# Performance work log

Measured on AMD Instinct MI355X. Metric: run time of the kernel, lower is better.

## Reference

```python
import jax, jax.numpy as jnp
import numpy as np

IN_SIZE = 4096
OUT_SIZE = 4096
BATCH = 256
NNZ = (IN_SIZE * OUT_SIZE) // 2


def setup_inputs() -> dict:
    key = jax.random.key(0)
    k_x, k_row, k_col, k_val = jax.random.split(key, 4)
    X = jax.random.normal(k_x, (BATCH, IN_SIZE), dtype=jnp.float32)
    rows = jax.random.randint(k_row, (NNZ,), 0, IN_SIZE, dtype=jnp.int64)
    cols = jax.random.randint(k_col, (NNZ,), 0, OUT_SIZE, dtype=jnp.int64)
    idx = jnp.stack([rows, cols], axis=1)  # [NNZ, 2] (input_idx, output_idx)
    lim = 1.0 / np.sqrt(IN_SIZE)
    val = jax.random.uniform(k_val, (NNZ,), dtype=jnp.float32, minval=-lim, maxval=lim)
    bias = jnp.zeros((OUT_SIZE,), dtype=jnp.float32)
    return {"X": X, "idx": idx, "val": val, "bias": bias}


def reference(X, idx, val, bias):
    # Scatter the COO sparse weight into a dense [IN, OUT] matrix.
    # .add accumulates duplicate indices, matching tf.SparseTensor matmul semantics.
    W = jnp.zeros((IN_SIZE, OUT_SIZE), dtype=val.dtype).at[idx[:, 0], idx[:, 1]].add(val)
    # Z = X @ W + b  (original: transpose(sparse_matmul(W^T, X^T)) + b)
    Z = jnp.dot(X, W) + bias
    return jax.nn.relu(Z)
```

## Files before the change

kernel.cpp:

```cpp
#include <hip/hip_runtime.h>
#include <hip/hip_bf16.h>

#define IN_SIZE 4096
#define OUT_SIZE 4096
#define BATCH 256
#define NNZ ((IN_SIZE * OUT_SIZE) / 2)

#define NB    512
#define BBIN  1024
#define EPB   (NNZ / BBIN)
#define CHUNK 4096
#define NCH   (EPB / CHUNK)
#define REP    8
#define SUBCAP 3072
#define CAP    (REP * SUBCAP)
#define SPLITK 4

#define BM 64
#define BN 64
#define BK 64
#define LDA 72

typedef float f32x4 __attribute__((ext_vector_type(4)));
typedef short s16x8 __attribute__((ext_vector_type(8)));

static const size_t OFF_XBF  = 0;
static const size_t OFF_WTBF = (size_t)2 << 20;
static const size_t OFF_PART = (size_t)34 << 20;
static const size_t OFF_BIN  = (size_t)50 << 20;
static const size_t OFF_CNT  = (size_t)98 << 20;
static const size_t WS_NEED  = OFF_CNT + (size_t)REP * NB * 4;

__device__ __forceinline__ short bfbits(float f) {
    __hip_bfloat16 h = __float2bfloat16(f);
    return __builtin_bit_cast(short, h);
}
__device__ __forceinline__ s16x8 pack8(f32x4 lo, f32x4 hi) {
    s16x8 r;
    r[0] = bfbits(lo[0]); r[1] = bfbits(lo[1]); r[2] = bfbits(lo[2]); r[3] = bfbits(lo[3]);
    r[4] = bfbits(hi[0]); r[5] = bfbits(hi[1]); r[6] = bfbits(hi[2]); r[7] = bfbits(hi[3]);
    return r;
}
__device__ __forceinline__ unsigned packel(int r, int c, float v) {
    return ((unsigned)(unsigned short)bfbits(v) << 15) |
           (unsigned)((c & 7) * IN_SIZE + r);
}
__device__ __forceinline__ float unpackv(unsigned p) {
    return __uint_as_float((p >> 15) << 16);
}

__device__ __forceinline__ void scan512(const unsigned* h, unsigned* out,
                                        unsigned* wsum, int t) {
    const int lane = t & 63, wid = t >> 6;
    const unsigned a0 = h[2 * t], a1 = h[2 * t + 1];
    const unsigned s = a0 + a1;
    unsigned inc = s;
#pragma unroll
    for (int d = 1; d < 64; d <<= 1) {
        const unsigned n = __shfl_up(inc, d);
        if (lane >= d) inc += n;
    }
    if (lane == 63) wsum[wid] = inc;
    __syncthreads();
    unsigned wpre = 0;
#pragma unroll
    for (int i = 0; i < 4; ++i)
        if (i < wid) wpre += wsum[i];
    const unsigned ex = wpre + inc - s;
    out[2 * t]     = ex;
    out[2 * t + 1] = ex + a0;
    __syncthreads();
}

__global__ __launch_bounds__(256) void k_xcvt(const float* __restrict__ X,
                                              s16x8* __restrict__ Xb) {
    const int i8 = blockIdx.x * 256 + threadIdx.x;
    const f32x4 lo = reinterpret_cast<const f32x4*>(X)[2 * i8];
    const f32x4 hi = reinterpret_cast<const f32x4*>(X)[2 * i8 + 1];
    Xb[i8] = pack8(lo, hi);
}

__global__ __launch_bounds__(256) void k_bin(const int4* __restrict__ idx4,
                                             const float2* __restrict__ val2,
                                             unsigned* __restrict__ cnt,
                                             unsigned* __restrict__ binned) {
    __shared__ unsigned hist[NB], start[NB], curb[NB], wsum[4];
    __shared__ uint2 st[CHUNK];
    const int t = threadIdx.x, blk = blockIdx.x;
    const int rep = blk & (REP - 1);

    for (int ch = 0; ch < NCH; ++ch) {
        hist[2 * t] = 0; hist[2 * t + 1] = 0;
        __syncthreads();
        const int pbase = (blk * EPB + ch * CHUNK) / 2;
        unsigned eb[16], er[16], epk[16];
#pragma unroll
        for (int j = 0; j < 8; ++j) {
            const int4 e   = idx4[pbase + t + 256 * j];
            const float2 v = val2[pbase + t + 256 * j];
            eb[2 * j]      = ((unsigned)e.y) >> 3;
            epk[2 * j]     = packel(e.x, e.y, v.x);
            er[2 * j]      = atomicAdd(&hist[eb[2 * j]], 1u);
            eb[2 * j + 1]  = ((unsigned)e.w) >> 3;
            epk[2 * j + 1] = packel(e.z, e.w, v.y);
            er[2 * j + 1]  = atomicAdd(&hist[eb[2 * j + 1]], 1u);
        }
        __syncthreads();
        scan512(hist, start, wsum, t);
        {
            const unsigned h0 = hist[2 * t], h1 = hist[2 * t + 1];
            const unsigned r0 = h0 ? atomicAdd(&cnt[rep * NB + 2 * t], h0) : 0u;
            const unsigned r1 = h1 ? atomicAdd(&cnt[rep * NB + 2 * t + 1], h1) : 0u;
            curb[2 * t]     = (unsigned)(2 * t) * CAP + rep * SUBCAP + r0;
            curb[2 * t + 1] = (unsigned)(2 * t + 1) * CAP + rep * SUBCAP + r1;
        }
        __syncthreads();
#pragma unroll
        for (int j = 0; j < 16; ++j) {
            const unsigned lp = start[eb[j]] + er[j];
            st[lp] = make_uint2(curb[eb[j]] + er[j], epk[j]);
        }
        __syncthreads();
#pragma unroll
        for (int j = 0; j < 16; ++j) {
            const uint2 s = st[t + 256 * j];
            binned[s.x] = s.y;
        }
        __syncthreads();
    }
}

__global__ __launch_bounds__(1024) void k_accum(const unsigned* __restrict__ binned,
                                                const unsigned* __restrict__ cnt,
                                                s16x8* __restrict__ Wtb8) {
    __shared__ float acc[8 * IN_SIZE];
    const int t = threadIdx.x, b = blockIdx.x;
    f32x4* a4 = reinterpret_cast<f32x4*>(acc);
#pragma unroll
    for (int j = 0; j < (8 * IN_SIZE / 4) / 1024; ++j)
        a4[t + 1024 * j] = (f32x4){0.f, 0.f, 0.f, 0.f};
    __syncthreads();
    const unsigned base = (unsigned)b * CAP;
#pragma unroll 1
    for (int r = 0; r < REP; ++r) {
        const unsigned n  = cnt[r * NB + b];
        const unsigned rb = base + r * SUBCAP;
        for (unsigned i = t; i < n; i += 1024) {
            const unsigned p = binned[rb + i];
            atomicAdd(&acc[p & 32767u], unpackv(p));
        }
    }
    __syncthreads();
    s16x8* dst = Wtb8 + (size_t)b * (8 * IN_SIZE / 8);
#pragma unroll
    for (int j = 0; j < (8 * IN_SIZE / 8) / 1024; ++j) {
        const int i8 = t + 1024 * j;
        dst[i8] = pack8(a4[2 * i8], a4[2 * i8 + 1]);
    }
}

__global__ __launch_bounds__(256) void k_gemm(const short* __restrict__ A,
                                              const short* __restrict__ B,
                                              float* __restrict__ part) {
    __shared__ short As[BM * LDA];
    __shared__ short Bs[BN * LDA];
    const int t  = threadIdx.x;
    const int l  = t & 63;
    const int w  = t >> 6;
    const int wm = (w >> 1) * 32, wn = (w & 1) * 32;
    const int lr = l & 15, kg = (l >> 4) * 8;
    const int bn = blockIdx.x * BN, bm = blockIdx.y * BM;
    const size_t kb = (size_t)blockIdx.z * (IN_SIZE / SPLITK);

    const int r0s = t >> 3;
    const int r1s = r0s + 32;
    const int c0  = (t & 7) * 8;
    const short* gA0 = A + (size_t)(bm + r0s) * IN_SIZE + kb + c0;
    const short* gA1 = A + (size_t)(bm + r1s) * IN_SIZE + kb + c0;
    const short* gB0 = B + (size_t)(bn + r0s) * IN_SIZE + kb + c0;
    const short* gB1 = B + (size_t)(bn + r1s) * IN_SIZE + kb + c0;

    f32x4 acc[2][2] = {};
    s16x8 ra0 = *reinterpret_cast<const s16x8*>(gA0);
    s16x8 ra1 = *reinterpret_cast<const s16x8*>(gA1);
    s16x8 rb0 = *reinterpret_cast<const s16x8*>(gB0);
    s16x8 rb1 = *reinterpret_cast<const s16x8*>(gB1);

    const int NIT = (IN_SIZE / SPLITK) / BK;
#pragma unroll 1
    for (int it = 0; it < NIT; ++it) {
        __syncthreads();
        *reinterpret_cast<s16x8*>(&As[r0s * LDA + c0]) = ra0;
        *reinterpret_cast<s16x8*>(&As[r1s * LDA + c0]) = ra1;
        *reinterpret_cast<s16x8*>(&Bs[r0s * LDA + c0]) = rb0;
        *reinterpret_cast<s16x8*>(&Bs[r1s * LDA + c0]) = rb1;
        __syncthreads();
        if (it + 1 < NIT) {
            const int o = (it + 1) * BK;
            ra0 = *reinterpret_cast<const s16x8*>(gA0 + o);
            ra1 = *reinterpret_cast<const s16x8*>(gA1 + o);
            rb0 = *reinterpret_cast<const s16x8*>(gB0 + o);
            rb1 = *reinterpret_cast<const s16x8*>(gB1 + o);
        }
        s16x8 af[2][2], bf[2][2];
#pragma unroll
        for (int kk = 0; kk < 2; ++kk) {
#pragma unroll
            for (int mi = 0; mi < 2; ++mi)
                af[kk][mi] = *reinterpret_cast<const s16x8*>(
                    &As[(wm + mi * 16 + lr) * LDA + kk * 32 + kg]);
#pragma unroll
            for (int ni = 0; ni < 2; ++ni)
                bf[kk][ni] = *reinterpret_cast<const s16x8*>(
                    &Bs[(wn + ni * 16 + lr) * LDA + kk * 32 + kg]);
        }
#pragma unroll
        for (int kk = 0; kk < 2; ++kk)
#pragma unroll
            for (int mi = 0; mi < 2; ++mi)
#pragma unroll
                for (int ni = 0; ni < 2; ++ni)
                    acc[mi][ni] = __builtin_amdgcn_mfma_f32_16x16x32_bf16(
                        af[kk][mi], bf[kk][ni], acc[mi][ni], 0, 0, 0);
    }

    float* P = part + (size_t)blockIdx.z * (BATCH * OUT_SIZE);
#pragma unroll
    for (int mi = 0; mi < 2; ++mi)
#pragma unroll
        for (int ni = 0; ni < 2; ++ni) {
            const int col = bn + wn + ni * 16 + lr;
            const int r0 = bm + wm + mi * 16 + ((l >> 4) << 2);
#pragma unroll
            for (int rr = 0; rr < 4; ++rr)
                P[(size_t)(r0 + rr) * OUT_SIZE + col] = acc[mi][ni][rr];
        }
}

__global__ __launch_bounds__(256) void k_reduce(const float* __restrict__ part,
                                                const float* __restrict__ bias,
                                                float* __restrict__ Z) {
    const int i4 = blockIdx.x * 256 + threadIdx.x;
    f32x4 s = reinterpret_cast<const f32x4*>(part)[i4];
#pragma unroll
    for (int r = 1; r < SPLITK; ++r) {
        const f32x4 p = reinterpret_cast<const f32x4*>(part + (size_t)r * BATCH * OUT_SIZE)[i4];
#pragma unroll
        for (int k = 0; k < 4; ++k) s[k] += p[k];
    }
    const f32x4 bv = reinterpret_cast<const f32x4*>(bias)[i4 & (OUT_SIZE / 4 - 1)];
    f32x4 o;
#pragma unroll
    for (int k = 0; k < 4; ++k) o[k] = fmaxf(s[k] + bv[k], 0.f);
    reinterpret_cast<f32x4*>(Z)[i4] = o;
}

#define SC_BLOCKS 1024
__global__ __launch_bounds__(256) void scatter_t(const int2* __restrict__ idx2,
                                                 const float* __restrict__ val,
                                                 float* __restrict__ Wt) {
    const int stride = SC_BLOCKS * 256;
    int i = blockIdx.x * 256 + threadIdx.x;
#pragma unroll 1
    for (int iter = 0; iter < NNZ / (4 * SC_BLOCKS * 256); ++iter) {
        const int2 e0 = idx2[i];
        const int2 e1 = idx2[i + stride];
        const int2 e2 = idx2[i + 2 * stride];
        const int2 e3 = idx2[i + 3 * stride];
        const float v0 = val[i], v1 = val[i + stride], v2 = val[i + 2 * stride], v3 = val[i + 3 * stride];
        atomicAdd(&Wt[e0.y * IN_SIZE + e0.x], v0);
        atomicAdd(&Wt[e1.y * IN_SIZE + e1.x], v1);
        atomicAdd(&Wt[e2.y * IN_SIZE + e2.x], v2);
        atomicAdd(&Wt[e3.y * IN_SIZE + e3.x], v3);
        i += 4 * stride;
    }
}

__global__ __launch_bounds__(256) void gemm_mfma(const float* __restrict__ X,
                                                 const float* __restrict__ Wt,
                                                 const float* __restrict__ bias,
                                                 float* __restrict__ Z) {
    const int l = threadIdx.x & 63, w = threadIdx.x >> 6;
    const int bm = blockIdx.y * 128, bn = blockIdx.x * 32;
    const int lr = l & 15, kg = (l >> 4) * 8;
    const float* pA[2];
    const float* pB[2];
#pragma unroll
    for (int mi = 0; mi < 2; ++mi) pA[mi] = X + (bm + w * 32 + mi * 16 + lr) * IN_SIZE + kg;
#pragma unroll
    for (int ni = 0; ni < 2; ++ni) pB[ni] = Wt + (bn + ni * 16 + lr) * IN_SIZE + kg;
    f32x4 acc[2][2] = {};
#pragma unroll 2
    for (int k0 = 0; k0 < IN_SIZE; k0 += 32) {
        s16x8 a[2], b[2];
#pragma unroll
        for (int mi = 0; mi < 2; ++mi) {
            const f32x4 lo = *reinterpret_cast<const f32x4*>(pA[mi]);
            const f32x4 hi = *reinterpret_cast<const f32x4*>(pA[mi] + 4);
            a[mi] = pack8(lo, hi); pA[mi] += 32;
        }
#pragma unroll
        for (int ni = 0; ni < 2; ++ni) {
            const f32x4 lo = *reinterpret_cast<const f32x4*>(pB[ni]);
            const f32x4 hi = *reinterpret_cast<const f32x4*>(pB[ni] + 4);
            b[ni] = pack8(lo, hi); pB[ni] += 32;
        }
#pragma unroll
        for (int mi = 0; mi < 2; ++mi)
#pragma unroll
            for (int ni = 0; ni < 2; ++ni)
                acc[mi][ni] = __builtin_amdgcn_mfma_f32_16x16x32_bf16(a[mi], b[ni], acc[mi][ni], 0, 0, 0);
    }
#pragma unroll
    for (int mi = 0; mi < 2; ++mi)
#pragma unroll
        for (int ni = 0; ni < 2; ++ni) {
            const int col = bn + ni * 16 + lr;
            const float bv = bias[col];
            const int r0 = bm + w * 32 + mi * 16 + ((l >> 4) << 2);
#pragma unroll
            for (int rr = 0; rr < 4; ++rr)
                Z[(r0 + rr) * OUT_SIZE + col] = fmaxf(acc[mi][ni][rr] + bv, 0.f);
        }
}

extern "C" void kernel_launch(void* const* d_in, const int* in_sizes, int n_in,
                              void* d_out, int out_size, void* d_ws, size_t ws_size,
                              hipStream_t stream) {
    const float* X    = (const float*)d_in[0];
    const int*   idx  = (const int*)d_in[1];
    const float* val  = (const float*)d_in[2];
    const float* bias = (const float*)d_in[3];
    float* Z = (float*)d_out;
    char*  ws = (char*)d_ws;

    if (ws_size >= WS_NEED) {
        s16x8*    Xb     = (s16x8*)(ws + OFF_XBF);
        short*    Wtb    = (short*)(ws + OFF_WTBF);
        float*    part   = (float*)(ws + OFF_PART);
        unsigned* binned = (unsigned*)(ws + OFF_BIN);
        unsigned* cnt    = (unsigned*)(ws + OFF_CNT);

        hipMemsetAsync(cnt, 0, (size_t)REP * NB * 4, stream);
        k_xcvt<<<(BATCH * IN_SIZE) / (256 * 8), 256, 0, stream>>>(X, Xb);
        k_bin<<<BBIN, 256, 0, stream>>>((const int4*)idx, (const float2*)val, cnt, binned);
        k_accum<<<NB, 1024, 0, stream>>>(binned, cnt, (s16x8*)Wtb);
        dim3 gg(OUT_SIZE / BN, BATCH / BM, SPLITK);
        k_gemm<<<gg, 256, 0, stream>>>((const short*)Xb, Wtb, part);
        k_reduce<<<(BATCH * OUT_SIZE) / (256 * 4), 256, 0, stream>>>(part, bias, Z);
    } else {
        float* Wt = (float*)d_ws;
        hipMemsetAsync(Wt, 0, (size_t)IN_SIZE * OUT_SIZE * sizeof(float), stream);
        scatter_t<<<SC_BLOCKS, 256, 0, stream>>>((const int2*)idx, val, Wt);
        dim3 grid(OUT_SIZE / 32, BATCH / 128);
        gemm_mfma<<<grid, 256, 0, stream>>>(X, Wt, bias, Z);
    }
}
```

Baseline: 227.3 us.

## Fuse X bf16 conversion into GEMM and double bin count with fixed-unroll accumulation

```diff
diff --git a/kernel.cpp b/kernel.cpp
--- a/kernel.cpp
+++ b/kernel.cpp
@@ -6,13 +6,14 @@
 #define BATCH 256
 #define NNZ ((IN_SIZE * OUT_SIZE) / 2)
 
-#define NB    512
+#define NB    1024
 #define BBIN  1024
+#define BTHR  512
 #define EPB   (NNZ / BBIN)
 #define CHUNK 4096
 #define NCH   (EPB / CHUNK)
 #define REP    8
-#define SUBCAP 3072
+#define SUBCAP 1536
 #define CAP    (REP * SUBCAP)
 #define SPLITK 4
 
@@ -24,11 +25,10 @@
 typedef float f32x4 __attribute__((ext_vector_type(4)));
 typedef short s16x8 __attribute__((ext_vector_type(8)));
 
-static const size_t OFF_XBF  = 0;
-static const size_t OFF_WTBF = (size_t)2 << 20;
-static const size_t OFF_PART = (size_t)34 << 20;
-static const size_t OFF_BIN  = (size_t)50 << 20;
-static const size_t OFF_CNT  = (size_t)98 << 20;
+static const size_t OFF_WTBF = 0;
+static const size_t OFF_PART = (size_t)32 << 20;
+static const size_t OFF_BIN  = (size_t)48 << 20;
+static const size_t OFF_CNT  = (size_t)96 << 20;
 static const size_t WS_NEED  = OFF_CNT + (size_t)REP * NB * 4;
 
 __device__ __forceinline__ short bfbits(float f) {
@@ -42,15 +42,15 @@
     return r;
 }
 __device__ __forceinline__ unsigned packel(int r, int c, float v) {
-    return ((unsigned)(unsigned short)bfbits(v) << 15) |
-           (unsigned)((c & 7) * IN_SIZE + r);
+    return ((unsigned)(unsigned short)bfbits(v) << 14) |
+           (unsigned)((c & 3) * IN_SIZE + r);
 }
 __device__ __forceinline__ float unpackv(unsigned p) {
-    return __uint_as_float((p >> 15) << 16);
-}
-
-__device__ __forceinline__ void scan512(const unsigned* h, unsigned* out,
-                                        unsigned* wsum, int t) {
+    return __uint_as_float((p >> 14) << 16);
+}
+
+__device__ __forceinline__ void scan1024(const unsigned* h, unsigned* out,
+                                         unsigned* wsum, int t) {
     const int lane = t & 63, wid = t >> 6;
     const unsigned a0 = h[2 * t], a1 = h[2 * t + 1];
     const unsigned s = a0 + a1;
@@ -64,7 +64,7 @@
     __syncthreads();
     unsigned wpre = 0;
 #pragma unroll
-    for (int i = 0; i < 4; ++i)
+    for (int i = 0; i < 8; ++i)
         if (i < wid) wpre += wsum[i];
     const unsigned ex = wpre + inc - s;
     out[2 * t]     = ex;
@@ -72,19 +72,11 @@
     __syncthreads();
 }
 
-__global__ __launch_bounds__(256) void k_xcvt(const float* __restrict__ X,
-                                              s16x8* __restrict__ Xb) {
-    const int i8 = blockIdx.x * 256 + threadIdx.x;
-    const f32x4 lo = reinterpret_cast<const f32x4*>(X)[2 * i8];
-    const f32x4 hi = reinterpret_cast<const f32x4*>(X)[2 * i8 + 1];
-    Xb[i8] = pack8(lo, hi);
-}
-
-__global__ __launch_bounds__(256) void k_bin(const int4* __restrict__ idx4,
-                                             const float2* __restrict__ val2,
-                                             unsigned* __restrict__ cnt,
-                                             unsigned* __restrict__ binned) {
-    __shared__ unsigned hist[NB], start[NB], curb[NB], wsum[4];
+__global__ __launch_bounds__(BTHR) void k_bin(const int4* __restrict__ idx4,
+                                              const float2* __restrict__ val2,
+                                              unsigned* __restrict__ cnt,
+                                              unsigned* __restrict__ binned) {
+    __shared__ unsigned hist[NB], start[NB], curb[NB], wsum[8];
     __shared__ uint2 st[CHUNK];
     const int t = threadIdx.x, blk = blockIdx.x;
     const int rep = blk & (REP - 1);
@@ -93,20 +85,20 @@
         hist[2 * t] = 0; hist[2 * t + 1] = 0;
         __syncthreads();
         const int pbase = (blk * EPB + ch * CHUNK) / 2;
-        unsigned eb[16], er[16], epk[16];
-#pragma unroll
-        for (int j = 0; j < 8; ++j) {
-            const int4 e   = idx4[pbase + t + 256 * j];
-            const float2 v = val2[pbase + t + 256 * j];
-            eb[2 * j]      = ((unsigned)e.y) >> 3;
+        unsigned eb[8], er[8], epk[8];
+#pragma unroll
+        for (int j = 0; j < 4; ++j) {
+            const int4 e   = idx4[pbase + t + BTHR * j];
+            const float2 v = val2[pbase + t + BTHR * j];
+            eb[2 * j]      = ((unsigned)e.y) >> 2;
             epk[2 * j]     = packel(e.x, e.y, v.x);
             er[2 * j]      = atomicAdd(&hist[eb[2 * j]], 1u);
-            eb[2 * j + 1]  = ((unsigned)e.w) >> 3;
+            eb[2 * j + 1]  = ((unsigned)e.w) >> 2;
             epk[2 * j + 1] = packel(e.z, e.w, v.y);
             er[2 * j + 1]  = atomicAdd(&hist[eb[2 * j + 1]], 1u);
         }
         __syncthreads();
-        scan512(hist, start, wsum, t);
+        scan1024(hist, start, wsum, t);
         {
             const unsigned h0 = hist[2 * t], h1 = hist[2 * t + 1];
             const unsigned r0 = h0 ? atomicAdd(&cnt[rep * NB + 2 * t], h0) : 0u;
@@ -116,14 +108,14 @@
         }
         __syncthreads();
 #pragma unroll
-        for (int j = 0; j < 16; ++j) {
+        for (int j = 0; j < 8; ++j) {
             const unsigned lp = start[eb[j]] + er[j];
             st[lp] = make_uint2(curb[eb[j]] + er[j], epk[j]);
         }
         __syncthreads();
 #pragma unroll
-        for (int j = 0; j < 16; ++j) {
-            const uint2 s = st[t + 256 * j];
+        for (int j = 0; j < 8; ++j) {
+            const uint2 s = st[t + BTHR * j];
             binned[s.x] = s.y;
         }
         __syncthreads();
@@ -133,33 +125,47 @@
 __global__ __launch_bounds__(1024) void k_accum(const unsigned* __restrict__ binned,
                                                 const unsigned* __restrict__ cnt,
                                                 s16x8* __restrict__ Wtb8) {
-    __shared__ float acc[8 * IN_SIZE];
+    __shared__ float acc[4 * IN_SIZE];
     const int t = threadIdx.x, b = blockIdx.x;
     f32x4* a4 = reinterpret_cast<f32x4*>(acc);
 #pragma unroll
-    for (int j = 0; j < (8 * IN_SIZE / 4) / 1024; ++j)
+    for (int j = 0; j < (4 * IN_SIZE / 4) / 1024; ++j)
         a4[t + 1024 * j] = (f32x4){0.f, 0.f, 0.f, 0.f};
     __syncthreads();
     const unsigned base = (unsigned)b * CAP;
-#pragma unroll 1
+    unsigned n[REP];
+#pragma unroll
     for (int r = 0; r < REP; ++r) {
-        const unsigned n  = cnt[r * NB + b];
-        const unsigned rb = base + r * SUBCAP;
-        for (unsigned i = t; i < n; i += 1024) {
-            const unsigned p = binned[rb + i];
-            atomicAdd(&acc[p & 32767u], unpackv(p));
-        }
-    }
+        const unsigned c = cnt[r * NB + b];
+        n[r] = c < SUBCAP ? c : SUBCAP;
+    }
+    unsigned p[REP]; bool v[REP];
+#pragma unroll
+    for (int r = 0; r < REP; ++r) {
+        v[r] = (unsigned)t < n[r];
+        p[r] = v[r] ? binned[base + r * SUBCAP + t] : 0u;
+    }
+#pragma unroll
+    for (int r = 0; r < REP; ++r)
+        if (v[r]) atomicAdd(&acc[p[r] & 16383u], unpackv(p[r]));
+#pragma unroll
+    for (int r = 0; r < REP; ++r) {
+        v[r] = (unsigned)(1024 + t) < n[r];
+        p[r] = v[r] ? binned[base + r * SUBCAP + 1024 + t] : 0u;
+    }
+#pragma unroll
+    for (int r = 0; r < REP; ++r)
+        if (v[r]) atomicAdd(&acc[p[r] & 16383u], unpackv(p[r]));
     __syncthreads();
-    s16x8* dst = Wtb8 + (size_t)b * (8 * IN_SIZE / 8);
-#pragma unroll
-    for (int j = 0; j < (8 * IN_SIZE / 8) / 1024; ++j) {
+    s16x8* dst = Wtb8 + (size_t)b * (4 * IN_SIZE / 8);
+#pragma unroll
+    for (int j = 0; j < (4 * IN_SIZE / 8) / 1024; ++j) {
         const int i8 = t + 1024 * j;
         dst[i8] = pack8(a4[2 * i8], a4[2 * i8 + 1]);
     }
 }
 
-__global__ __launch_bounds__(256) void k_gemm(const short* __restrict__ A,
+__global__ __launch_bounds__(256) void k_gemm(const float* __restrict__ X,
                                               const short* __restrict__ B,
                                               float* __restrict__ part) {
     __shared__ short As[BM * LDA];
@@ -175,32 +181,36 @@
     const int r0s = t >> 3;
     const int r1s = r0s + 32;
     const int c0  = (t & 7) * 8;
-    const short* gA0 = A + (size_t)(bm + r0s) * IN_SIZE + kb + c0;
-    const short* gA1 = A + (size_t)(bm + r1s) * IN_SIZE + kb + c0;
+    const float* gA0 = X + (size_t)(bm + r0s) * IN_SIZE + kb + c0;
+    const float* gA1 = X + (size_t)(bm + r1s) * IN_SIZE + kb + c0;
     const short* gB0 = B + (size_t)(bn + r0s) * IN_SIZE + kb + c0;
     const short* gB1 = B + (size_t)(bn + r1s) * IN_SIZE + kb + c0;
 
     f32x4 acc[2][2] = {};
-    s16x8 ra0 = *reinterpret_cast<const s16x8*>(gA0);
-    s16x8 ra1 = *reinterpret_cast<const s16x8*>(gA1);
-    s16x8 rb0 = *reinterpret_cast<const s16x8*>(gB0);
-    s16x8 rb1 = *reinterpret_cast<const s16x8*>(gB1);
+    f32x4 a0lo = *reinterpret_cast<const f32x4*>(gA0);
+    f32x4 a0hi = *reinterpret_cast<const f32x4*>(gA0 + 4);
+    f32x4 a1lo = *reinterpret_cast<const f32x4*>(gA1);
+    f32x4 a1hi = *reinterpret_cast<const f32x4*>(gA1 + 4);
+    s16x8 rb0  = *reinterpret_cast<const s16x8*>(gB0);
+    s16x8 rb1  = *reinterpret_cast<const s16x8*>(gB1);
 
     const int NIT = (IN_SIZE / SPLITK) / BK;
 #pragma unroll 1
     for (int it = 0; it < NIT; ++it) {
         __syncthreads();
-        *reinterpret_cast<s16x8*>(&As[r0s * LDA + c0]) = ra0;
-        *reinterpret_cast<s16x8*>(&As[r1s * LDA + c0]) = ra1;
+        *reinterpret_cast<s16x8*>(&As[r0s * LDA + c0]) = pack8(a0lo, a0hi);
+        *reinterpret_cast<s16x8*>(&As[r1s * LDA + c0]) = pack8(a1lo, a1hi);
         *reinterpret_cast<s16x8*>(&Bs[r0s * LDA + c0]) = rb0;
         *reinterpret_cast<s16x8*>(&Bs[r1s * LDA + c0]) = rb1;
         __syncthreads();
         if (it + 1 < NIT) {
             const int o = (it + 1) * BK;
-            ra0 = *reinterpret_cast<const s16x8*>(gA0 + o);
-            ra1 = *reinterpret_cast<const s16x8*>(gA1 + o);
-            rb0 = *reinterpret_cast<const s16x8*>(gB0 + o);
-            rb1 = *reinterpret_cast<const s16x8*>(gB1 + o);
+            a0lo = *reinterpret_cast<const f32x4*>(gA0 + o);
+            a0hi = *reinterpret_cast<const f32x4*>(gA0 + o + 4);
+            a1lo = *reinterpret_cast<const f32x4*>(gA1 + o);
+            a1hi = *reinterpret_cast<const f32x4*>(gA1 + o + 4);
+            rb0  = *reinterpret_cast<const s16x8*>(gB0 + o);
+            rb1  = *reinterpret_cast<const s16x8*>(gB1 + o);
         }
         s16x8 af[2][2], bf[2][2];
 #pragma unroll
@@ -335,18 +345,16 @@
     char*  ws = (char*)d_ws;
 
     if (ws_size >= WS_NEED) {
-        s16x8*    Xb     = (s16x8*)(ws + OFF_XBF);
         short*    Wtb    = (short*)(ws + OFF_WTBF);
         float*    part   = (float*)(ws + OFF_PART);
         unsigned* binned = (unsigned*)(ws + OFF_BIN);
         unsigned* cnt    = (unsigned*)(ws + OFF_CNT);
 
         hipMemsetAsync(cnt, 0, (size_t)REP * NB * 4, stream);
-        k_xcvt<<<(BATCH * IN_SIZE) / (256 * 8), 256, 0, stream>>>(X, Xb);
-        k_bin<<<BBIN, 256, 0, stream>>>((const int4*)idx, (const float2*)val, cnt, binned);
+        k_bin<<<BBIN, BTHR, 0, stream>>>((const int4*)idx, (const float2*)val, cnt, binned);
         k_accum<<<NB, 1024, 0, stream>>>(binned, cnt, (s16x8*)Wtb);
         dim3 gg(OUT_SIZE / BN, BATCH / BM, SPLITK);
-        k_gemm<<<gg, 256, 0, stream>>>((const short*)Xb, Wtb, part);
+        k_gemm<<<gg, 256, 0, stream>>>(X, Wtb, part);
         k_reduce<<<(BATCH * OUT_SIZE) / (256 * 4), 256, 0, stream>>>(part, bias, Z);
     } else {
         float* Wt = (float*)d_ws;
```

Result: slower. 239.1 us (+5.2%).
